# Optimization experiments

Hardware: AMD Instinct MI355X
Metric: run time of the kernel (lower is better)

The kernel has to match this reference:

```python
import jax, jax.numpy as jnp
import numpy as np

C = 0.01            # curvature, hard-coded in the original forward
TEMPERATURE = 0.5
SCALE_BY_TEMPERATURE = True
ARTANH_CLAMP = 1.0 - 1e-5


def setup_inputs() -> dict:
    key = jax.random.key(0)
    k1, k2 = jax.random.split(key)
    B, D = 4096, 128
    features = jax.random.uniform(k1, (B, D), dtype=jnp.float32)
    labels = jax.random.randint(k2, (B,), 0, 32, dtype=jnp.int64)
    return {"features": features, "labels": labels}


def _pairwise_hyp_distance(features):
    # Pair [i, j] in the original: mobius_add(x=-features[j], y=features[i], c)
    # mobius_add(x, y) = (a*x + b*y) / den with
    #   a = 1 + 2c<x,y> + c||y||^2,  b = 1 - c||x||^2,
    #   den = 1 + 2c<x,y> + c^2 ||x||^2 ||y||^2
    # ||a*x + b*y||^2 = a^2||x||^2 + 2ab<x,y> + b^2||y||^2, so the full
    # (B,B,D) broadcast collapses to Gram-matrix algebra (identical math).
    G = features @ features.T                 # [B,B], <f_i, f_j>
    sq = jnp.sum(features * features, axis=-1)  # [B], ||f||^2
    xy = -G                                    # <x,y> with x=-f_j, y=f_i
    x2 = sq[None, :]                           # ||f_j||^2
    y2 = sq[:, None]                           # ||f_i||^2
    a = 1.0 + 2.0 * C * xy + C * y2
    b = 1.0 - C * x2
    den = 1.0 + 2.0 * C * xy + (C * C) * x2 * y2
    num_sq = jnp.maximum(a * a * x2 + 2.0 * a * b * xy + b * b * y2, 0.0)
    norm_diff = jnp.sqrt(C * num_sq) / jnp.abs(den)   # ||sqrt(c)*mobius_add||
    norm_diff = jnp.clip(norm_diff, 0.0, ARTANH_CLAMP)
    return jnp.arctanh(norm_diff) * (2.0 / np.sqrt(C))  # [B,B]


def reference(features, labels):
    B = features.shape[0]
    dist = _pairwise_hyp_distance(features)
    anchor_dot_contrast = -dist / TEMPERATURE
    logits_max = jax.lax.stop_gradient(jnp.max(anchor_dot_contrast, axis=1, keepdims=True))
    logits = anchor_dot_contrast - logits_max
    exp_logits = jnp.exp(logits)

    mask = (labels[:, None] == labels[None, :]).astype(jnp.float32)
    logits_mask = 1.0 - jnp.eye(B, dtype=jnp.float32)
    positives_mask = mask * logits_mask
    negatives_mask = 1.0 - mask

    num_pos = jnp.sum(positives_mask, axis=1)          # [B]
    valid = (num_pos > 0).astype(jnp.float32)
    denominator = (jnp.sum(exp_logits * negatives_mask, axis=1, keepdims=True)
                   + jnp.sum(exp_logits * positives_mask, axis=1, keepdims=True))
    log_probs = logits - jnp.log(denominator)

    row_loss = -jnp.sum(log_probs * positives_mask, axis=1) / jnp.maximum(num_pos, 1.0)
    if SCALE_BY_TEMPERATURE:
        row_loss = row_loss * TEMPERATURE
    row_loss = jnp.where(jnp.isnan(row_loss), 0.0, row_loss)
    n_valid = jnp.sum(valid)
    loss = jnp.sum(row_loss * valid) / jnp.maximum(n_valid, 1.0)
    return loss
```

## Files before the change

kernel.cpp:

```cpp
#include <hip/hip_runtime.h>
#include <cstddef>


typedef __bf16 bf16x8 __attribute__((ext_vector_type(8)));
typedef __bf16 bf16x4 __attribute__((ext_vector_type(4)));
typedef float  f32x4  __attribute__((ext_vector_type(4)));

#define C_CONST 0.01f
#define RATIO_MIN 5.000025e-06f
#define LOGIT_SCALE 13.86294361119890619f
#define TEMP 0.5f
#define LN2 0.69314718055994530942f
constexpr int DD = 128;

__global__ __launch_bounds__(256) void prep_kernel(
    const float* __restrict__ F, __bf16* __restrict__ Fh, float* __restrict__ sq,
    float* __restrict__ denom, float* __restrict__ possum, float* __restrict__ npos) {
  const int tid = threadIdx.x;
  const int lane = tid & 31;
  const int row = blockIdx.x * 8 + (tid >> 5);
  const float4 v = *reinterpret_cast<const float4*>(F + (size_t)row * DD + lane * 4);
  float s = v.x * v.x + v.y * v.y + v.z * v.z + v.w * v.w;
  bf16x4 h;
  h[0] = (__bf16)v.x; h[1] = (__bf16)v.y; h[2] = (__bf16)v.z; h[3] = (__bf16)v.w;
  *reinterpret_cast<bf16x4*>(Fh + (size_t)row * DD + lane * 4) = h;
#pragma unroll
  for (int off = 1; off < 32; off <<= 1) s += __shfl_xor(s, off);
  if (lane == 0) { sq[row] = s; denom[row] = 0.f; possum[row] = 0.f; npos[row] = 0.f; }
}

__global__ __launch_bounds__(256, 4) void gram_kernel(
    const __bf16* __restrict__ Fh,
    const float* __restrict__ sq, const int* __restrict__ labels,
    float* __restrict__ denom, float* __restrict__ possum, float* __restrict__ npos,
    int B) {
  __shared__ __bf16 Bs[128 * 128];
  __shared__ float colAcc[4][3][128];
  char* BsB = reinterpret_cast<char*>(Bs);

  const int tid = threadIdx.x;
  const int l  = tid & 63;
  const int w  = tid >> 6;
  const int lg = l >> 4, ln = l & 15;
  const int lx = ln & 7;

  const int t = blockIdx.x;
  int bj = (int)((sqrtf((float)(4 * t + 1)) - 1.f) * 0.5f);
  while (bj * bj + bj > t) --bj;
  while ((bj + 1) * (bj + 1) + (bj + 1) <= t) ++bj;
  const int bi = t - (bj * bj + bj);

  const int row0 = bi * 64 + w * 16;
  const int col0 = bj * 128;

#pragma unroll
  for (int j = 0; j < 8; ++j) {
    const int k = tid + j * 256;
    const int row = k >> 4;
    const int cc = (k & 15) ^ (row & 7);
    bf16x8 v = *reinterpret_cast<const bf16x8*>(Fh + (size_t)(col0 + row) * DD + cc * 8);
    *reinterpret_cast<bf16x8*>(BsB + (size_t)k * 16) = v;
  }

  const __bf16* Ahp = Fh + (size_t)(row0 + ln) * DD + lg * 8;
  bf16x8 ah[4];
#pragma unroll
  for (int kt = 0; kt < 4; ++kt)
    ah[kt] = *reinterpret_cast<const bf16x8*>(Ahp + kt * 32);

  float si[4]; int li[4];
#pragma unroll
  for (int r = 0; r < 4; ++r) {
    const int row = row0 + lg * 4 + r;
    si[r] = sq[row];
    li[r] = labels[row];
  }
  float sqj[8]; int labj[8];
#pragma unroll
  for (int fj = 0; fj < 8; ++fj) {
    sqj[fj]  = sq[col0 + fj * 16 + ln];
    labj[fj] = labels[col0 + fj * 16 + ln];
  }

  __syncthreads();

  float dacc[4] = {}, pacc[4] = {}, nacc[4] = {};

#pragma unroll
  for (int fj = 0; fj < 8; ++fj) {
    const int rbase = (fj * 16 + ln) * 256;
    bf16x8 bh[4];
#pragma unroll
    for (int kt = 0; kt < 4; ++kt)
      bh[kt] = *reinterpret_cast<const bf16x8*>(BsB + rbase + ((((kt * 4 + lg) ^ lx)) << 4));

    f32x4 acc = (f32x4){0.f, 0.f, 0.f, 0.f};
#pragma unroll
    for (int kt = 0; kt < 4; ++kt)
      acc = __builtin_amdgcn_mfma_f32_16x16x32_bf16(ah[kt], bh[kt], acc, 0, 0, 0);

    const int col = col0 + fj * 16 + ln;
    const float sjv = sqj[fj];
    const int   ljv = labj[fj];
    const float qv = C_CONST * sjv;
    const float b  = 1.f - qv;
    const float b2 = b * b;
    float cd = 0.f, cp = 0.f, cn = 0.f;
#pragma unroll
    for (int r = 0; r < 4; ++r) {
      const int row = row0 + lg * 4 + r;
      const float g   = acc[r];
      const float pi_ = C_CONST * si[r];
      const float tt  = fmaf(-2.f * C_CONST, g, 1.f);
      const float a   = tt + pi_;
      const float den = fabsf(fmaf(pi_, qv, tt));
      float ns = a * a * sjv;
      ns = fmaf(b2, si[r], ns);
      ns = fmaf(-2.f * a * b, g, ns);
      ns = fmaxf(ns, 0.f);
      const float rr = __builtin_amdgcn_sqrtf(C_CONST * ns);
      float ratio = (den - rr) * __builtin_amdgcn_rcpf(den + rr);
      ratio = fmaxf(ratio, RATIO_MIN);
      const float P = __builtin_amdgcn_logf(ratio);
      const float t2 = ratio * ratio;
      const float t4 = t2 * t2;
      const float t5 = t4 * ratio;
      const float t10 = t5 * t5;
      const float e = t10 * t10;
      const bool mask = row < col;
      const bool same = mask && (ljv == li[r]);
      const float ev = mask ? e : 0.f;
      const float pv = same ? LOGIT_SCALE * P : 0.f;
      const float nv = same ? 1.f : 0.f;
      dacc[r] += ev; pacc[r] += pv; nacc[r] += nv;
      cd += ev; cp += pv; cn += nv;
    }
    cd += __shfl_xor(cd, 16); cd += __shfl_xor(cd, 32);
    cp += __shfl_xor(cp, 16); cp += __shfl_xor(cp, 32);
    cn += __shfl_xor(cn, 16); cn += __shfl_xor(cn, 32);
    if (l < 16) {
      colAcc[w][0][fj * 16 + ln] = cd;
      colAcc[w][1][fj * 16 + ln] = cp;
      colAcc[w][2][fj * 16 + ln] = cn;
    }
  }

#pragma unroll
  for (int r = 0; r < 4; ++r) {
    float d = dacc[r], p = pacc[r], n = nacc[r];
#pragma unroll
    for (int off = 1; off < 16; off <<= 1) {
      d += __shfl_xor(d, off);
      p += __shfl_xor(p, off);
      n += __shfl_xor(n, off);
    }
    if (ln == 0) {
      const int row = row0 + lg * 4 + r;
      atomicAdd(&denom[row], d);
      atomicAdd(&possum[row], p);
      atomicAdd(&npos[row], n);
    }
  }

  __syncthreads();
  if (tid < 128) {
    const float d = colAcc[0][0][tid] + colAcc[1][0][tid] + colAcc[2][0][tid] + colAcc[3][0][tid];
    const float p = colAcc[0][1][tid] + colAcc[1][1][tid] + colAcc[2][1][tid] + colAcc[3][1][tid];
    const float n = colAcc[0][2][tid] + colAcc[1][2][tid] + colAcc[2][2][tid] + colAcc[3][2][tid];
    atomicAdd(&denom[col0 + tid], d);
    atomicAdd(&possum[col0 + tid], p);
    atomicAdd(&npos[col0 + tid], n);
  }
}

__global__ __launch_bounds__(1024) void finalize_kernel(
    const float* __restrict__ denom, const float* __restrict__ possum,
    const float* __restrict__ npos, float* __restrict__ out, int B) {
  float s_loss = 0.f, s_valid = 0.f;
#pragma unroll
  for (int j = 0; j < 4; ++j) {
    const int i = threadIdx.x + j * 1024;
    const float n = npos[i];
    const float d = denom[i];
    const float p = possum[i];
    if (n > 0.f) {
      float ln_d = __builtin_amdgcn_logf(d) * LN2;
      float rl = -(p - n * ln_d) / n * TEMP;
      if (!(rl != rl)) s_loss += rl;
      s_valid += 1.f;
    }
  }
#pragma unroll
  for (int off = 1; off < 64; off <<= 1) {
    s_loss += __shfl_xor(s_loss, off);
    s_valid += __shfl_xor(s_valid, off);
  }
  __shared__ float red[32];
  const int wid = threadIdx.x >> 6;
  if ((threadIdx.x & 63) == 0) { red[wid] = s_loss; red[wid + 16] = s_valid; }
  __syncthreads();
  if (threadIdx.x == 0) {
    float L = 0.f, V = 0.f;
#pragma unroll
    for (int i = 0; i < 16; ++i) { L += red[i]; V += red[i + 16]; }
    out[0] = L / fmaxf(V, 1.f);
  }
}

extern "C" void kernel_launch(void* const* d_in, const int* in_sizes, int n_in,
                              void* d_out, int out_size, void* d_ws, size_t ws_size,
                              hipStream_t stream) {
  const float* F = (const float*)d_in[0];
  const int* labels = (const int*)d_in[1];
  const int B = in_sizes[1];

  float* sq     = (float*)d_ws;
  float* denom  = sq + B;
  float* possum = denom + B;
  float* npos   = possum + B;
  __bf16* Fh = (__bf16*)(npos + B);

  const int nbj = B / 128;
  const int nblocks = nbj * nbj + nbj;

  prep_kernel<<<dim3(B / 8), dim3(256), 0, stream>>>(F, Fh, sq, denom, possum, npos);
  gram_kernel<<<dim3(nblocks), dim3(256), 0, stream>>>(
      Fh, sq, labels, denom, possum, npos, B);
  finalize_kernel<<<1, dim3(1024), 0, stream>>>(denom, possum, npos, (float*)d_out, B);
}
```

Measured before the change: 40.49 us.

## Fuse finalize into gram kernel via last-block counter and software-pipeline LDS loads

Removes the separate finalize kernel launch: each gram block bumps a global counter after a threadfence, and the last block to finish performs the loss reduction using atomic loads. The counter is zeroed in prep_kernel. The per-column-tile loop is also manually unrolled with double-buffered LDS fragment loads, and the four MFMAs are split into two independent accumulation chains to shorten dependency latency. This trades one launch for a serialized tail reduction run by a single 256-thread block, plus possibly higher register pressure.

```diff
diff --git a/kernel.cpp b/kernel.cpp
--- a/kernel.cpp
+++ b/kernel.cpp
@@ -15,10 +15,12 @@
 
 __global__ __launch_bounds__(256) void prep_kernel(
     const float* __restrict__ F, __bf16* __restrict__ Fh, float* __restrict__ sq,
-    float* __restrict__ denom, float* __restrict__ possum, float* __restrict__ npos) {
+    float* __restrict__ denom, float* __restrict__ possum, float* __restrict__ npos,
+    unsigned int* __restrict__ cnt) {
   const int tid = threadIdx.x;
   const int lane = tid & 31;
   const int row = blockIdx.x * 8 + (tid >> 5);
+  if (blockIdx.x == 0 && tid == 0) *cnt = 0u;
   const float4 v = *reinterpret_cast<const float4*>(F + (size_t)row * DD + lane * 4);
   float s = v.x * v.x + v.y * v.y + v.z * v.z + v.w * v.w;
   bf16x4 h;
@@ -33,7 +35,8 @@
     const __bf16* __restrict__ Fh,
     const float* __restrict__ sq, const int* __restrict__ labels,
     float* __restrict__ denom, float* __restrict__ possum, float* __restrict__ npos,
-    int B) {
+    unsigned int* __restrict__ cnt, float* __restrict__ out,
+    int B, int nblocks) {
   __shared__ __bf16 Bs[128 * 128];
   __shared__ float colAcc[4][3][128];
   char* BsB = reinterpret_cast<char*>(Bs);
@@ -63,10 +66,10 @@
   }
 
   const __bf16* Ahp = Fh + (size_t)(row0 + ln) * DD + lg * 8;
-  bf16x8 ah[4];
-#pragma unroll
-  for (int kt = 0; kt < 4; ++kt)
-    ah[kt] = *reinterpret_cast<const bf16x8*>(Ahp + kt * 32);
+  bf16x8 ah0 = *reinterpret_cast<const bf16x8*>(Ahp);
+  bf16x8 ah1 = *reinterpret_cast<const bf16x8*>(Ahp + 32);
+  bf16x8 ah2 = *reinterpret_cast<const bf16x8*>(Ahp + 64);
+  bf16x8 ah3 = *reinterpret_cast<const bf16x8*>(Ahp + 96);
 
   float si[4]; int li[4];
 #pragma unroll
@@ -82,68 +85,90 @@
     labj[fj] = labels[col0 + fj * 16 + ln];
   }
 
+  const int o0 = ((0 * 4 + lg) ^ lx) << 4;
+  const int o1 = ((1 * 4 + lg) ^ lx) << 4;
+  const int o2 = ((2 * 4 + lg) ^ lx) << 4;
+  const int o3 = ((3 * 4 + lg) ^ lx) << 4;
+
   __syncthreads();
 
   float dacc[4] = {}, pacc[4] = {}, nacc[4] = {};
 
-#pragma unroll
-  for (int fj = 0; fj < 8; ++fj) {
-    const int rbase = (fj * 16 + ln) * 256;
-    bf16x8 bh[4];
-#pragma unroll
-    for (int kt = 0; kt < 4; ++kt)
-      bh[kt] = *reinterpret_cast<const bf16x8*>(BsB + rbase + ((((kt * 4 + lg) ^ lx)) << 4));
-
-    f32x4 acc = (f32x4){0.f, 0.f, 0.f, 0.f};
-#pragma unroll
-    for (int kt = 0; kt < 4; ++kt)
-      acc = __builtin_amdgcn_mfma_f32_16x16x32_bf16(ah[kt], bh[kt], acc, 0, 0, 0);
-
-    const int col = col0 + fj * 16 + ln;
-    const float sjv = sqj[fj];
-    const int   ljv = labj[fj];
-    const float qv = C_CONST * sjv;
-    const float b  = 1.f - qv;
-    const float b2 = b * b;
-    float cd = 0.f, cp = 0.f, cn = 0.f;
-#pragma unroll
-    for (int r = 0; r < 4; ++r) {
-      const int row = row0 + lg * 4 + r;
-      const float g   = acc[r];
-      const float pi_ = C_CONST * si[r];
-      const float tt  = fmaf(-2.f * C_CONST, g, 1.f);
-      const float a   = tt + pi_;
-      const float den = fabsf(fmaf(pi_, qv, tt));
-      float ns = a * a * sjv;
-      ns = fmaf(b2, si[r], ns);
-      ns = fmaf(-2.f * a * b, g, ns);
-      ns = fmaxf(ns, 0.f);
-      const float rr = __builtin_amdgcn_sqrtf(C_CONST * ns);
-      float ratio = (den - rr) * __builtin_amdgcn_rcpf(den + rr);
-      ratio = fmaxf(ratio, RATIO_MIN);
-      const float P = __builtin_amdgcn_logf(ratio);
-      const float t2 = ratio * ratio;
-      const float t4 = t2 * t2;
-      const float t5 = t4 * ratio;
-      const float t10 = t5 * t5;
-      const float e = t10 * t10;
-      const bool mask = row < col;
-      const bool same = mask && (ljv == li[r]);
-      const float ev = mask ? e : 0.f;
-      const float pv = same ? LOGIT_SCALE * P : 0.f;
-      const float nv = same ? 1.f : 0.f;
-      dacc[r] += ev; pacc[r] += pv; nacc[r] += nv;
-      cd += ev; cp += pv; cn += nv;
-    }
-    cd += __shfl_xor(cd, 16); cd += __shfl_xor(cd, 32);
-    cp += __shfl_xor(cp, 16); cp += __shfl_xor(cp, 32);
-    cn += __shfl_xor(cn, 16); cn += __shfl_xor(cn, 32);
-    if (l < 16) {
-      colAcc[w][0][fj * 16 + ln] = cd;
-      colAcc[w][1][fj * 16 + ln] = cp;
-      colAcc[w][2][fj * 16 + ln] = cn;
-    }
-  }
+#define LOADB(P0, P1, P2, P3, FJ) do {                                   \
+    const int rb_ = ((FJ) * 16 + ln) * 256;                              \
+    P0 = *reinterpret_cast<const bf16x8*>(BsB + rb_ + o0);               \
+    P1 = *reinterpret_cast<const bf16x8*>(BsB + rb_ + o1);               \
+    P2 = *reinterpret_cast<const bf16x8*>(BsB + rb_ + o2);               \
+    P3 = *reinterpret_cast<const bf16x8*>(BsB + rb_ + o3);               \
+  } while (0)
+
+#define DO_FJ(FJ, C0, C1, C2, C3) do {                                   \
+    f32x4 x_ = (f32x4){0.f, 0.f, 0.f, 0.f};                              \
+    f32x4 y_ = (f32x4){0.f, 0.f, 0.f, 0.f};                              \
+    x_ = __builtin_amdgcn_mfma_f32_16x16x32_bf16(ah0, C0, x_, 0, 0, 0);  \
+    y_ = __builtin_amdgcn_mfma_f32_16x16x32_bf16(ah2, C2, y_, 0, 0, 0);  \
+    x_ = __builtin_amdgcn_mfma_f32_16x16x32_bf16(ah1, C1, x_, 0, 0, 0);  \
+    y_ = __builtin_amdgcn_mfma_f32_16x16x32_bf16(ah3, C3, y_, 0, 0, 0);  \
+    const f32x4 acc_ = x_ + y_;                                          \
+    const int col = col0 + (FJ) * 16 + ln;                               \
+    const float sjv = sqj[FJ];                                           \
+    const int   ljv = labj[FJ];                                          \
+    const float qv = C_CONST * sjv;                                      \
+    const float bb = 1.f - qv;                                           \
+    const float b2 = bb * bb;                                            \
+    float cd = 0.f, cp = 0.f, cn = 0.f;                                  \
+    _Pragma("unroll")                                                    \
+    for (int r = 0; r < 4; ++r) {                                        \
+      const int row = row0 + lg * 4 + r;                                 \
+      const float g   = acc_[r];                                         \
+      const float pi_ = C_CONST * si[r];                                 \
+      const float tt  = fmaf(-2.f * C_CONST, g, 1.f);                    \
+      const float aa  = tt + pi_;                                        \
+      const float den = fabsf(fmaf(pi_, qv, tt));                        \
+      float ns = aa * aa * sjv;                                          \
+      ns = fmaf(b2, si[r], ns);                                          \
+      ns = fmaf(-2.f * aa * bb, g, ns);                                  \
+      ns = fmaxf(ns, 0.f);                                               \
+      const float rr = __builtin_amdgcn_sqrtf(C_CONST * ns);             \
+      float ratio = (den - rr) * __builtin_amdgcn_rcpf(den + rr);        \
+      ratio = fmaxf(ratio, RATIO_MIN);                                   \
+      const float P = __builtin_amdgcn_logf(ratio);                      \
+      const float t2_ = ratio * ratio;                                   \
+      const float t4_ = t2_ * t2_;                                       \
+      const float t5_ = t4_ * ratio;                                     \
+      const float t10_ = t5_ * t5_;                                      \
+      const float e = t10_ * t10_;                                       \
+      const bool mask = row < col;                                       \
+      const bool same = mask && (ljv == li[r]);                          \
+      const float ev = mask ? e : 0.f;                                   \
+      const float pv = same ? LOGIT_SCALE * P : 0.f;                     \
+      const float nv = same ? 1.f : 0.f;                                 \
+      dacc[r] += ev; pacc[r] += pv; nacc[r] += nv;                       \
+      cd += ev; cp += pv; cn += nv;                                      \
+    }                                                                    \
+    cd += __shfl_xor(cd, 16); cd += __shfl_xor(cd, 32);                  \
+    cp += __shfl_xor(cp, 16); cp += __shfl_xor(cp, 32);                  \
+    cn += __shfl_xor(cn, 16); cn += __shfl_xor(cn, 32);                  \
+    if (l < 16) {                                                        \
+      colAcc[w][0][(FJ) * 16 + ln] = cd;                                 \
+      colAcc[w][1][(FJ) * 16 + ln] = cp;                                 \
+      colAcc[w][2][(FJ) * 16 + ln] = cn;                                 \
+    }                                                                    \
+  } while (0)
+
+  bf16x8 a0_, a1_, a2_, a3_, b0_, b1_, b2_, b3_;
+  LOADB(a0_, a1_, a2_, a3_, 0);
+  LOADB(b0_, b1_, b2_, b3_, 1); DO_FJ(0, a0_, a1_, a2_, a3_);
+  LOADB(a0_, a1_, a2_, a3_, 2); DO_FJ(1, b0_, b1_, b2_, b3_);
+  LOADB(b0_, b1_, b2_, b3_, 3); DO_FJ(2, a0_, a1_, a2_, a3_);
+  LOADB(a0_, a1_, a2_, a3_, 4); DO_FJ(3, b0_, b1_, b2_, b3_);
+  LOADB(b0_, b1_, b2_, b3_, 5); DO_FJ(4, a0_, a1_, a2_, a3_);
+  LOADB(a0_, a1_, a2_, a3_, 6); DO_FJ(5, b0_, b1_, b2_, b3_);
+  LOADB(b0_, b1_, b2_, b3_, 7); DO_FJ(6, a0_, a1_, a2_, a3_);
+  DO_FJ(7, b0_, b1_, b2_, b3_);
+
+#undef LOADB
+#undef DO_FJ
 
 #pragma unroll
   for (int r = 0; r < 4; ++r) {
@@ -171,39 +196,38 @@
     atomicAdd(&possum[col0 + tid], p);
     atomicAdd(&npos[col0 + tid], n);
   }
-}
-
-__global__ __launch_bounds__(1024) void finalize_kernel(
-    const float* __restrict__ denom, const float* __restrict__ possum,
-    const float* __restrict__ npos, float* __restrict__ out, int B) {
-  float s_loss = 0.f, s_valid = 0.f;
-#pragma unroll
-  for (int j = 0; j < 4; ++j) {
-    const int i = threadIdx.x + j * 1024;
-    const float n = npos[i];
-    const float d = denom[i];
-    const float p = possum[i];
-    if (n > 0.f) {
-      float ln_d = __builtin_amdgcn_logf(d) * LN2;
-      float rl = -(p - n * ln_d) / n * TEMP;
-      if (!(rl != rl)) s_loss += rl;
-      s_valid += 1.f;
-    }
-  }
-#pragma unroll
-  for (int off = 1; off < 64; off <<= 1) {
-    s_loss += __shfl_xor(s_loss, off);
-    s_valid += __shfl_xor(s_valid, off);
-  }
-  __shared__ float red[32];
-  const int wid = threadIdx.x >> 6;
-  if ((threadIdx.x & 63) == 0) { red[wid] = s_loss; red[wid + 16] = s_valid; }
+
+  __threadfence();
+  __shared__ unsigned int lastFlag;
+  if (tid == 0)
+    lastFlag = (atomicAdd(cnt, 1u) == (unsigned)(nblocks - 1)) ? 1u : 0u;
   __syncthreads();
-  if (threadIdx.x == 0) {
-    float L = 0.f, V = 0.f;
-#pragma unroll
-    for (int i = 0; i < 16; ++i) { L += red[i]; V += red[i + 16]; }
-    out[0] = L / fmaxf(V, 1.f);
+  if (lastFlag != 0u) {
+    float s_loss = 0.f, s_valid = 0.f;
+    for (int i = tid; i < B; i += 256) {
+      const float n = __hip_atomic_load(&npos[i],  __ATOMIC_RELAXED, __HIP_MEMORY_SCOPE_AGENT);
+      const float d = __hip_atomic_load(&denom[i], __ATOMIC_RELAXED, __HIP_MEMORY_SCOPE_AGENT);
+      const float p = __hip_atomic_load(&possum[i],__ATOMIC_RELAXED, __HIP_MEMORY_SCOPE_AGENT);
+      if (n > 0.f) {
+        const float ln_d = __builtin_amdgcn_logf(d) * LN2;
+        const float rl = -(p - n * ln_d) / n * TEMP;
+        if (!(rl != rl)) s_loss += rl;
+        s_valid += 1.f;
+      }
+    }
+#pragma unroll
+    for (int off = 1; off < 64; off <<= 1) {
+      s_loss += __shfl_xor(s_loss, off);
+      s_valid += __shfl_xor(s_valid, off);
+    }
+    __shared__ float red[8];
+    if ((tid & 63) == 0) { red[w] = s_loss; red[w + 4] = s_valid; }
+    __syncthreads();
+    if (tid == 0) {
+      const float L = red[0] + red[1] + red[2] + red[3];
+      const float V = red[4] + red[5] + red[6] + red[7];
+      out[0] = L / fmaxf(V, 1.f);
+    }
   }
 }
 
@@ -218,13 +242,13 @@
   float* denom  = sq + B;
   float* possum = denom + B;
   float* npos   = possum + B;
-  __bf16* Fh = (__bf16*)(npos + B);
+  unsigned int* cnt = (unsigned int*)(npos + B);
+  __bf16* Fh = (__bf16*)(cnt + 64);
 
   const int nbj = B / 128;
   const int nblocks = nbj * nbj + nbj;
 
-  prep_kernel<<<dim3(B / 8), dim3(256), 0, stream>>>(F, Fh, sq, denom, possum, npos);
+  prep_kernel<<<dim3(B / 8), dim3(256), 0, stream>>>(F, Fh, sq, denom, possum, npos, cnt);
   gram_kernel<<<dim3(nblocks), dim3(256), 0, stream>>>(
-      Fh, sq, labels, denom, possum, npos, B);
-  finalize_kernel<<<1, dim3(1024), 0, stream>>>(denom, possum, npos, (float*)d_out, B);
+      Fh, sq, labels, denom, possum, npos, cnt, (float*)d_out, B, nblocks);
 }
```

Measured after the change: 115.3 us. 2.85x slower.
